# Kernel tuning notes

Hardware: AMD Instinct MI355X
Metric: run time of the kernel (lower is better)

Reference implementation:

```python
import jax, jax.numpy as jnp
import numpy as np

HEAD_SIZE = 64
NUM_HEADS = 16
D_MODEL = HEAD_SIZE * NUM_HEADS
BATCH = 2
SEQ = 2048


def setup_inputs() -> dict:
    key = jax.random.key(0)
    ks = jax.random.split(key, 9)
    s = 1.0 / np.sqrt(D_MODEL)
    inp = {
        "hidden_states": jax.random.normal(ks[0], (BATCH, SEQ, D_MODEL), jnp.float32),
        "Wq": jax.random.uniform(ks[1], (D_MODEL, D_MODEL), jnp.float32, -s, s),
        "bq": jax.random.uniform(ks[2], (D_MODEL,), jnp.float32, -s, s),
        "Wk": jax.random.uniform(ks[3], (D_MODEL, D_MODEL), jnp.float32, -s, s),
        "bk": jax.random.uniform(ks[4], (D_MODEL,), jnp.float32, -s, s),
        "Wv": jax.random.uniform(ks[5], (D_MODEL, D_MODEL), jnp.float32, -s, s),
        "bv": jax.random.uniform(ks[6], (D_MODEL,), jnp.float32, -s, s),
        "Wo": jax.random.uniform(ks[7], (D_MODEL, D_MODEL), jnp.float32, -s, s),
        "bo": jax.random.uniform(ks[8], (D_MODEL,), jnp.float32, -s, s),
    }
    return inp


def _split_heads(x):
    # [B, S, H*D] -> [B, H, S, D]
    b, s, _ = x.shape
    return x.reshape(b, s, NUM_HEADS, HEAD_SIZE).transpose(0, 2, 1, 3)


def reference(hidden_states, Wq, bq, Wk, bk, Wv, bv, Wo, bo):
    q = _split_heads(hidden_states @ Wq + bq)  # [B,H,S,D]
    k = _split_heads(hidden_states @ Wk + bk)
    v = _split_heads(hidden_states @ Wv + bv)
    scale = 1.0 / jnp.sqrt(jnp.asarray(HEAD_SIZE, hidden_states.dtype))
    scores = jnp.einsum("bhqd,bhkd->bhqk", q, k) * scale  # [B,H,S,S]
    weights = jax.nn.softmax(scores, axis=-1)
    attended = jnp.einsum("bhqk,bhkd->bhqd", weights, v)  # [B,H,S,D]
    merged = attended.transpose(0, 2, 1, 3).reshape(hidden_states.shape)  # [B,S,H*D]
    return merged @ Wo + bo
```

## Files before the change

kernel.cpp:

```cpp
#include <hip/hip_runtime.h>
#include <hip/hip_bf16.h>

#define D_MODEL 1024
#define HEADS 16
#define HSZ 64
#define BATCH 2
#define SEQ 2048
#define TOK (BATCH*SEQ)
#define NT (SEQ/64)

typedef __attribute__((ext_vector_type(8))) short bf16x8;
typedef __attribute__((ext_vector_type(4))) float f32x4;

#define QSCALE 0.1803368801111244f
#define THR_L2 11.541560327f

static __device__ __forceinline__ unsigned short f2bf(float f) {
  union { float f; unsigned u; } v; v.f = f;
  unsigned r = v.u + 0x7fffu + ((v.u >> 16) & 1u);
  return (unsigned short)(r >> 16);
}

static __device__ __forceinline__ float exp2_fast(float x) {
  float r;
  asm("v_exp_f32 %0, %1" : "=v"(r) : "v"(x));
  return r;
}

static __device__ __forceinline__ unsigned cvt_pk_bf16(float a, float b) {
  unsigned r;
  asm("v_cvt_pk_bf16_f32 %0, %1, %2" : "=v"(r) : "v"(a), "v"(b));
  return r;
}

static __device__ __forceinline__ int swz128(int row, int g) {
  return ((row << 7) + (g << 4)) ^ ((row & 7) << 4);
}

static __device__ __forceinline__ int xs4(int lr) {
  return ((lr & 7) << 1) | (lr >> 3);
}

static __device__ __forceinline__ void load_lds16(const void* g, void* l) {
  __builtin_amdgcn_global_load_lds(
      (const __attribute__((address_space(1))) unsigned*)g,
      (__attribute__((address_space(3))) unsigned*)l, 16, 0, 0);
}


__global__ void cvt_bf16_kernel(const float* __restrict__ src,
                                unsigned short* __restrict__ dst, int n) {
  int i = (blockIdx.x * blockDim.x + threadIdx.x) * 8;
  if (i >= n) return;
  float4 v0 = *reinterpret_cast<const float4*>(src + i);
  float4 v1 = *reinterpret_cast<const float4*>(src + i + 4);
  ushort4 o0, o1;
  o0.x = f2bf(v0.x); o0.y = f2bf(v0.y); o0.z = f2bf(v0.z); o0.w = f2bf(v0.w);
  o1.x = f2bf(v1.x); o1.y = f2bf(v1.y); o1.z = f2bf(v1.z); o1.w = f2bf(v1.w);
  *reinterpret_cast<ushort4*>(dst + i) = o0;
  *reinterpret_cast<ushort4*>(dst + i + 4) = o1;
}

__global__ void transpose_cvt_kernel(const float* __restrict__ Wq, const float* __restrict__ Wk,
                                     const float* __restrict__ Wv, const float* __restrict__ Wo,
                                     unsigned short* __restrict__ Wqkvt,
                                     unsigned short* __restrict__ Wot) {
  __shared__ float tile[32][33];
  int m = blockIdx.z;
  const float* src = (m == 0) ? Wq : (m == 1) ? Wk : (m == 2) ? Wv : Wo;
  unsigned short* dst = (m < 3) ? (Wqkvt + (size_t)m * D_MODEL * D_MODEL) : Wot;
  int i0 = blockIdx.y * 32, o0 = blockIdx.x * 32;
  int tx = threadIdx.x, ty = threadIdx.y;
  for (int k = 0; k < 32; k += 8)
    tile[ty + k][tx] = src[(size_t)(i0 + ty + k) * D_MODEL + o0 + tx];
  __syncthreads();
  for (int k = 0; k < 32; k += 8)
    dst[(size_t)(o0 + ty + k) * D_MODEL + i0 + tx] = f2bf(tile[tx][ty + k]);
}


template<int EPI>
__global__ __launch_bounds__(256) void gemm128_kernel(
    const unsigned short* __restrict__ A, const unsigned short* __restrict__ Bt,
    int K, int N,
    const float* __restrict__ b0, const float* __restrict__ b1, const float* __restrict__ b2,
    unsigned short* __restrict__ Qb, unsigned short* __restrict__ Kb,
    unsigned short* __restrict__ Vtb, float* __restrict__ Cout)
{
  __shared__ char As[128 * 64];
  __shared__ char Bs[128 * 64];
  int gx = gridDim.x;
  int orig = blockIdx.y * gx + blockIdx.x;
  int chunk = (gx * gridDim.y) >> 3;
  int sw = (orig & 7) * chunk + (orig >> 3);
  int m0 = (sw / gx) * 128, n0 = (sw % gx) * 128;
  int tid = threadIdx.x;
  int wv = tid >> 6, l = tid & 63;
  int wm = wv >> 1, wn = wv & 1;
  int lg = l >> 4, lr = l & 15;
  int srow = wv * 32 + (l >> 2);
  int scol = (l & 3) * 8;

  f32x4 acc[4][4];
#pragma unroll
  for (int i = 0; i < 4; i++)
#pragma unroll
    for (int j = 0; j < 4; j++) acc[i][j] = (f32x4){0.f, 0.f, 0.f, 0.f};

  for (int k0 = 0; k0 < K; k0 += 32) {
    __syncthreads();
    const unsigned short* ga = A  + (size_t)(m0 + srow) * K + k0 + scol;
    const unsigned short* gb = Bt + (size_t)(n0 + srow) * K + k0 + scol;
    load_lds16(ga,                       As + wv * 2048);
    load_lds16(ga + (size_t)16 * K,      As + wv * 2048 + 1024);
    load_lds16(gb,                       Bs + wv * 2048);
    load_lds16(gb + (size_t)16 * K,      Bs + wv * 2048 + 1024);
    __syncthreads();

    bf16x8 af[4], bfv[4];
#pragma unroll
    for (int mi = 0; mi < 4; mi++)
      af[mi] = *reinterpret_cast<const bf16x8*>(As + (wm * 64 + mi * 16 + lr) * 64 + lg * 16);
#pragma unroll
    for (int ni = 0; ni < 4; ni++)
      bfv[ni] = *reinterpret_cast<const bf16x8*>(Bs + (wn * 64 + ni * 16 + lr) * 64 + lg * 16);
#pragma unroll
    for (int mi = 0; mi < 4; mi++)
#pragma unroll
      for (int ni = 0; ni < 4; ni++)
        acc[mi][ni] = __builtin_amdgcn_mfma_f32_16x16x32_bf16(af[mi], bfv[ni], acc[mi][ni], 0, 0, 0);
  }

#pragma unroll
  for (int mi = 0; mi < 4; mi++) {
    int gr0 = m0 + wm * 64 + mi * 16 + lg * 4;
#pragma unroll
    for (int ni = 0; ni < 4; ni++) {
      int gc = n0 + wn * 64 + ni * 16 + lr;
      if (EPI == 0) {
        int mat = gc >> 10, o = gc & 1023;
        int hh = o >> 6, d = o & 63;
        const float* bias = (mat == 0) ? b0 : (mat == 1) ? b1 : b2;
        float bv = bias[o];
#pragma unroll
        for (int r = 0; r < 4; r++) {
          int t = gr0 + r;
          int b = t >> 11, s = t & 2047;
          float v = acc[mi][ni][r] + bv;
          if (mat == 0) v *= QSCALE;
          unsigned short u = f2bf(v);
          size_t head = (size_t)(b * HEADS + hh);
          if (mat == 0)
            Qb[(head * SEQ + s) * HSZ + d] = u;
          else if (mat == 1)
            Kb[((head * SEQ + s) * HSZ + d) ^ ((s & 7) << 3)] = u;
          else
            Vtb[(((head * HSZ + d) * SEQ + s)) ^ ((d & 7) << 3)] = u;
        }
      } else {
        float bv = b0[gc];
#pragma unroll
        for (int r = 0; r < 4; r++) {
          int t = gr0 + r;
          Cout[(size_t)t * N + gc] = acc[mi][ni][r] + bv;
        }
      }
    }
  }
}


#define KOFF(c) ((c) * 8192)
#define VOFF(c) (16384 + (c) * 8192)
#define POFF(w) (32768 + (w) * 2048)

__global__ __launch_bounds__(512, 4) void attn_kernel(
    const unsigned short* __restrict__ Qb, const unsigned short* __restrict__ Kb,
    const unsigned short* __restrict__ Vtb, unsigned short* __restrict__ Mg)
{
  __shared__ char lds[49152];

  int orig = blockIdx.y * 16 + blockIdx.x;
  int swzb = (orig & 7) * 64 + (orig >> 3);
  int bh = swzb >> 4;
  int q0 = (swzb & 15) * 128;
  int b = bh >> 4, h = bh & 15;
  int tid = threadIdx.x, w = tid >> 6, l = tid & 63;
  int lg = l >> 4, lr = l & 15;
  const unsigned short* Qh = Qb + (size_t)bh * SEQ * HSZ;
  const char* Kg = (const char*)(Kb + (size_t)bh * SEQ * HSZ) + (size_t)tid * 16;
  const char* Vg = (const char*)(Vtb + (size_t)bh * HSZ * SEQ)
                   + (size_t)(tid >> 3) * (SEQ * 2) + (tid & 7) * 16;

  int dsb[2] = { swz128(lr, lg), swz128(lr, lg + 4) };
  int pwa[4], paa[4];
#pragma unroll
  for (int ni = 0; ni < 4; ni++)
    pwa[ni] = POFF(w) + (lr << 7) + ((((ni << 2) + lg) ^ xs4(lr)) << 3);
#pragma unroll
  for (int k2 = 0; k2 < 2; k2++)
#pragma unroll
    for (int hh = 0; hh < 2; hh++)
      paa[k2 * 2 + hh] = POFF(w) + (lr << 7) + (((k2 * 8 + lg * 2 + hh) ^ xs4(lr)) << 3);

  bf16x8 qf2[2];
#pragma unroll
  for (int k2 = 0; k2 < 2; k2++)
    qf2[k2] = *reinterpret_cast<const bf16x8*>(
        Qh + (size_t)(q0 + w * 16 + lr) * HSZ + k2 * 32 + lg * 8);

  f32x4 of[4];
  f32x4 lones = (f32x4){0.f, 0.f, 0.f, 0.f};
#pragma unroll
  for (int ni = 0; ni < 4; ni++) of[ni] = (f32x4){0.f, 0.f, 0.f, 0.f};
  float m_r = -1e30f;

  bf16x8 vone;
#pragma unroll
  for (int j = 0; j < 8; j++) vone[j] = (short)0x3F80;

  auto stage = [&](int t, int nb) {
    if (t < NT) {
      load_lds16(Kg + (size_t)t * 8192, lds + KOFF(nb) + w * 1024);
      load_lds16(Vg + (size_t)t * 128,  lds + VOFF(nb) + w * 1024);
    }
  };

  auto body = [&](int t, int cur) {
    stage(t + 1, cur ^ 1);

    f32x4 sf[4];
#pragma unroll
    for (int ni = 0; ni < 4; ni++) {
      sf[ni] = (f32x4){0.f, 0.f, 0.f, 0.f};
#pragma unroll
      for (int k2 = 0; k2 < 2; k2++) {
        bf16x8 kf = *reinterpret_cast<const bf16x8*>(lds + dsb[k2] + KOFF(cur) + ni * 2048);
        sf[ni] = __builtin_amdgcn_mfma_f32_16x16x32_bf16(kf, qf2[k2], sf[ni], 0, 0, 0);
      }
    }

    float lm = fmaxf(fmaxf(fmaxf(sf[0][0], sf[0][1]), fmaxf(sf[0][2], sf[0][3])),
                     fmaxf(fmaxf(sf[1][0], sf[1][1]), fmaxf(sf[1][2], sf[1][3])));
    lm = fmaxf(lm,
         fmaxf(fmaxf(fmaxf(sf[2][0], sf[2][1]), fmaxf(sf[2][2], sf[2][3])),
               fmaxf(fmaxf(sf[3][0], sf[3][1]), fmaxf(sf[3][2], sf[3][3]))));

    if (__any(lm > m_r + THR_L2)) {
      float vm = fmaxf(lm, __shfl_xor(lm, 16));
      vm = fmaxf(vm, __shfl_xor(vm, 32));
      float mn = fmaxf(m_r, vm);
      float al = exp2_fast(m_r - mn);
      m_r = mn;
#pragma unroll
      for (int r = 0; r < 4; r++) {
        float a = __shfl(al, lg * 4 + r, 16);
        lones[r] *= a;
#pragma unroll
        for (int ni = 0; ni < 4; ni++) of[ni][r] *= a;
      }
    }

#pragma unroll
    for (int ni = 0; ni < 4; ni++) {
      uint2 pw;
      pw.x = cvt_pk_bf16(exp2_fast(sf[ni][0] - m_r), exp2_fast(sf[ni][1] - m_r));
      pw.y = cvt_pk_bf16(exp2_fast(sf[ni][2] - m_r), exp2_fast(sf[ni][3] - m_r));
      *reinterpret_cast<uint2*>(lds + pwa[ni]) = pw;
    }

    bf16x8 pa[2];
#pragma unroll
    for (int k2 = 0; k2 < 2; k2++) {
      uint2 lo = *reinterpret_cast<const uint2*>(lds + paa[k2 * 2]);
      uint2 hi = *reinterpret_cast<const uint2*>(lds + paa[k2 * 2 + 1]);
      int4 tt = {(int)lo.x, (int)lo.y, (int)hi.x, (int)hi.y};
      pa[k2] = *reinterpret_cast<bf16x8*>(&tt);
    }

    __builtin_amdgcn_s_setprio(1);
#pragma unroll
    for (int k2 = 0; k2 < 2; k2++)
      lones = __builtin_amdgcn_mfma_f32_16x16x32_bf16(pa[k2], vone, lones, 0, 0, 0);
#pragma unroll
    for (int ni = 0; ni < 4; ni++)
#pragma unroll
      for (int k2 = 0; k2 < 2; k2++) {
        bf16x8 vf = *reinterpret_cast<const bf16x8*>(lds + dsb[k2] + VOFF(cur) + ni * 2048);
        of[ni] = __builtin_amdgcn_mfma_f32_16x16x32_bf16(pa[k2], vf, of[ni], 0, 0, 0);
      }
    __builtin_amdgcn_s_setprio(0);

    __syncthreads();
  };

  stage(0, 0);
  __syncthreads();
  for (int kt = 0; kt < NT; kt += 2) {
    body(kt, 0);
    body(kt + 1, 1);
  }

#pragma unroll
  for (int r = 0; r < 4; r++) {
    float inv = 1.0f / lones[r];
    int q = q0 + w * 16 + lg * 4 + r;
#pragma unroll
    for (int ni = 0; ni < 4; ni++) {
      int dm = h * 64 + ni * 16 + lr;
      Mg[(size_t)(b * SEQ + q) * D_MODEL + dm] = f2bf(of[ni][r] * inv);
    }
  }
}


extern "C" void kernel_launch(void* const* d_in, const int* in_sizes, int n_in,
                              void* d_out, int out_size, void* d_ws, size_t ws_size,
                              hipStream_t stream) {
  const float* X  = (const float*)d_in[0];
  const float* Wq = (const float*)d_in[1];
  const float* bq = (const float*)d_in[2];
  const float* Wk = (const float*)d_in[3];
  const float* bk = (const float*)d_in[4];
  const float* Wv = (const float*)d_in[5];
  const float* bv = (const float*)d_in[6];
  const float* Wo = (const float*)d_in[7];
  const float* bo = (const float*)d_in[8];
  float* out = (float*)d_out;

  char* ws = (char*)d_ws;
  unsigned short* Xbf   = (unsigned short*)(ws);
  unsigned short* Wqkvt = (unsigned short*)(ws + ((size_t)8  << 20));
  unsigned short* Wot   = (unsigned short*)(ws + ((size_t)14 << 20));
  unsigned short* Qb    = (unsigned short*)(ws + ((size_t)16 << 20));
  unsigned short* Kb    = (unsigned short*)(ws + ((size_t)24 << 20));
  unsigned short* Vtb   = (unsigned short*)(ws + ((size_t)32 << 20));
  unsigned short* Mg = Xbf;

  cvt_bf16_kernel<<<(TOK * D_MODEL / 8 + 255) / 256, 256, 0, stream>>>(X, Xbf, TOK * D_MODEL);
  transpose_cvt_kernel<<<dim3(32, 32, 4), dim3(32, 8), 0, stream>>>(Wq, Wk, Wv, Wo, Wqkvt, Wot);
  gemm128_kernel<0><<<dim3(24, 32), 256, 0, stream>>>(Xbf, Wqkvt, 1024, 3072,
                                                      bq, bk, bv, Qb, Kb, Vtb, nullptr);
  attn_kernel<<<dim3(16, 32), 512, 0, stream>>>(Qb, Kb, Vtb, Mg);
  gemm128_kernel<1><<<dim3(8, 32), 256, 0, stream>>>(Mg, Wot, 1024, 1024,
                                                     bo, nullptr, nullptr,
                                                     nullptr, nullptr, nullptr, out);
}
```

Before: 203.7 us.

## Specialize QKV and projection GEMMs with K=64 XOR-swizzled tiles and staged V transpose

Splits the templated GEMM into a QKV kernel and an output-projection kernel. Both now load K-depth 64 per iteration into XOR-swizzled LDS to cut bank conflicts and halve barrier count. The QKV kernel stages the V tile through LDS so V^T is written with 16-byte coalesced stores instead of scattered 2-byte ones. The projection kernel uses 128x64 tiles for more blocks. This trades extra LDS and added complexity for better memory efficiency in both GEMMs.

```diff
diff --git a/kernel.cpp b/kernel.cpp
--- a/kernel.cpp
+++ b/kernel.cpp
@@ -79,16 +79,15 @@
 }
 
 
-template<int EPI>
-__global__ __launch_bounds__(256) void gemm128_kernel(
+__global__ __launch_bounds__(256, 3) void gemm_qkv_kernel(
     const unsigned short* __restrict__ A, const unsigned short* __restrict__ Bt,
-    int K, int N,
     const float* __restrict__ b0, const float* __restrict__ b1, const float* __restrict__ b2,
     unsigned short* __restrict__ Qb, unsigned short* __restrict__ Kb,
-    unsigned short* __restrict__ Vtb, float* __restrict__ Cout)
+    unsigned short* __restrict__ Vtb)
 {
-  __shared__ char As[128 * 64];
-  __shared__ char Bs[128 * 64];
+  __shared__ char As[16384];
+  __shared__ char Bs[16384];
+  const int K = D_MODEL;
   int gx = gridDim.x;
   int orig = blockIdx.y * gx + blockIdx.x;
   int chunk = (gx * gridDim.y) >> 3;
@@ -98,8 +97,16 @@
   int wv = tid >> 6, l = tid & 63;
   int wm = wv >> 1, wn = wv & 1;
   int lg = l >> 4, lr = l & 15;
-  int srow = wv * 32 + (l >> 2);
-  int scol = (l & 3) * 8;
+
+  int sr = wv * 32 + (l >> 3);
+  int csw = ((l & 7) ^ (l >> 3)) << 3;
+  const unsigned short* gaA = A  + (size_t)(m0 + sr) * K + csw;
+  const unsigned short* gaB = Bt + (size_t)(n0 + sr) * K + csw;
+
+  int gk0 = ((lg       ^ (lr & 7)) << 4);
+  int gk1 = (((4 + lg) ^ (lr & 7)) << 4);
+  int arow = (wm * 64 + lr) * 128;
+  int brow = (wn * 64 + lr) * 128;
 
   f32x4 acc[4][4];
 #pragma unroll
@@ -107,41 +114,45 @@
 #pragma unroll
     for (int j = 0; j < 4; j++) acc[i][j] = (f32x4){0.f, 0.f, 0.f, 0.f};
 
-  for (int k0 = 0; k0 < K; k0 += 32) {
-    __syncthreads();
-    const unsigned short* ga = A  + (size_t)(m0 + srow) * K + k0 + scol;
-    const unsigned short* gb = Bt + (size_t)(n0 + srow) * K + k0 + scol;
-    load_lds16(ga,                       As + wv * 2048);
-    load_lds16(ga + (size_t)16 * K,      As + wv * 2048 + 1024);
-    load_lds16(gb,                       Bs + wv * 2048);
-    load_lds16(gb + (size_t)16 * K,      Bs + wv * 2048 + 1024);
-    __syncthreads();
-
-    bf16x8 af[4], bfv[4];
+  for (int k0 = 0; k0 < K; k0 += 64) {
+    __syncthreads();
+#pragma unroll
+    for (int i = 0; i < 4; i++) {
+      load_lds16(gaA + k0 + i * 8 * K, As + wv * 4096 + i * 1024);
+      load_lds16(gaB + k0 + i * 8 * K, Bs + wv * 4096 + i * 1024);
+    }
+    __syncthreads();
+
+    bf16x8 af0[4], af1[4], bf0[4], bf1[4];
+#pragma unroll
+    for (int mi = 0; mi < 4; mi++) {
+      af0[mi] = *reinterpret_cast<const bf16x8*>(As + arow + mi * 2048 + gk0);
+      af1[mi] = *reinterpret_cast<const bf16x8*>(As + arow + mi * 2048 + gk1);
+    }
+#pragma unroll
+    for (int ni = 0; ni < 4; ni++) {
+      bf0[ni] = *reinterpret_cast<const bf16x8*>(Bs + brow + ni * 2048 + gk0);
+      bf1[ni] = *reinterpret_cast<const bf16x8*>(Bs + brow + ni * 2048 + gk1);
+    }
 #pragma unroll
     for (int mi = 0; mi < 4; mi++)
-      af[mi] = *reinterpret_cast<const bf16x8*>(As + (wm * 64 + mi * 16 + lr) * 64 + lg * 16);
-#pragma unroll
-    for (int ni = 0; ni < 4; ni++)
-      bfv[ni] = *reinterpret_cast<const bf16x8*>(Bs + (wn * 64 + ni * 16 + lr) * 64 + lg * 16);
-#pragma unroll
-    for (int mi = 0; mi < 4; mi++)
-#pragma unroll
-      for (int ni = 0; ni < 4; ni++)
-        acc[mi][ni] = __builtin_amdgcn_mfma_f32_16x16x32_bf16(af[mi], bfv[ni], acc[mi][ni], 0, 0, 0);
-  }
-
-#pragma unroll
-  for (int mi = 0; mi < 4; mi++) {
-    int gr0 = m0 + wm * 64 + mi * 16 + lg * 4;
-#pragma unroll
-    for (int ni = 0; ni < 4; ni++) {
-      int gc = n0 + wn * 64 + ni * 16 + lr;
-      if (EPI == 0) {
+#pragma unroll
+      for (int ni = 0; ni < 4; ni++) {
+        acc[mi][ni] = __builtin_amdgcn_mfma_f32_16x16x32_bf16(af0[mi], bf0[ni], acc[mi][ni], 0, 0, 0);
+        acc[mi][ni] = __builtin_amdgcn_mfma_f32_16x16x32_bf16(af1[mi], bf1[ni], acc[mi][ni], 0, 0, 0);
+      }
+  }
+
+  if (n0 < 2048) {
+#pragma unroll
+    for (int mi = 0; mi < 4; mi++) {
+      int gr0 = m0 + wm * 64 + mi * 16 + lg * 4;
+#pragma unroll
+      for (int ni = 0; ni < 4; ni++) {
+        int gc = n0 + wn * 64 + ni * 16 + lr;
         int mat = gc >> 10, o = gc & 1023;
         int hh = o >> 6, d = o & 63;
-        const float* bias = (mat == 0) ? b0 : (mat == 1) ? b1 : b2;
-        float bv = bias[o];
+        float bv = (mat == 0) ? b0[o] : b1[o];
 #pragma unroll
         for (int r = 0; r < 4; r++) {
           int t = gr0 + r;
@@ -152,19 +163,140 @@
           size_t head = (size_t)(b * HEADS + hh);
           if (mat == 0)
             Qb[(head * SEQ + s) * HSZ + d] = u;
-          else if (mat == 1)
+          else
             Kb[((head * SEQ + s) * HSZ + d) ^ ((s & 7) << 3)] = u;
-          else
-            Vtb[(((head * HSZ + d) * SEQ + s)) ^ ((d & 7) << 3)] = u;
         }
-      } else {
-        float bv = b0[gc];
-#pragma unroll
-        for (int r = 0; r < 4; r++) {
-          int t = gr0 + r;
-          Cout[(size_t)t * N + gc] = acc[mi][ni][r] + bv;
+      }
+    }
+  } else {
+    int bglob = m0 >> 11;
+    int hh0 = (n0 - 2048) >> 6;
+    float bvv[4];
+#pragma unroll
+    for (int ni = 0; ni < 4; ni++) bvv[ni] = b2[(n0 - 2048) + wn * 64 + ni * 16 + lr];
+
+    __syncthreads();
+    {
+      char* dstbuf = (wm == 0) ? As : Bs;
+#pragma unroll
+      for (int mi = 0; mi < 4; mi++) {
+        int lrow = mi * 16 + lg * 4;
+#pragma unroll
+        for (int ni = 0; ni < 4; ni++) {
+          int cc = wn * 64 + ni * 16 + lr;
+          uint2 pw;
+          pw.x = cvt_pk_bf16(acc[mi][ni][0] + bvv[ni], acc[mi][ni][1] + bvv[ni]);
+          pw.y = cvt_pk_bf16(acc[mi][ni][2] + bvv[ni], acc[mi][ni][3] + bvv[ni]);
+          int ba = (cc * 128 + lrow * 2) ^ ((cc & 7) << 3);
+          *reinterpret_cast<uint2*>(dstbuf + ba) = pw;
         }
       }
+    }
+    __syncthreads();
+    int ck = tid & 7;
+#pragma unroll
+    for (int pass = 0; pass < 4; ++pass) {
+      int cc = (tid >> 3) + pass * 32;
+      int x = cc & 7;
+      int d = cc & 63, hh = hh0 + (cc >> 6);
+      size_t rowbase = (((size_t)(bglob * HEADS + hh)) * HSZ + d) * SEQ;
+      int slo = ((ck * 2)     ^ x) << 3;
+      int shi = ((ck * 2 + 1) ^ x) << 3;
+      {
+        uint2 lo = *reinterpret_cast<const uint2*>(As + (cc << 7) + slo);
+        uint2 hi = *reinterpret_cast<const uint2*>(As + (cc << 7) + shi);
+        int s = (m0 & 2047) + ck * 8;
+        size_t idx = (rowbase + s) ^ ((d & 7) << 3);
+        uint4 val = {lo.x, lo.y, hi.x, hi.y};
+        *reinterpret_cast<uint4*>(Vtb + idx) = val;
+      }
+      {
+        uint2 lo = *reinterpret_cast<const uint2*>(Bs + (cc << 7) + slo);
+        uint2 hi = *reinterpret_cast<const uint2*>(Bs + (cc << 7) + shi);
+        int s = (m0 & 2047) + 64 + ck * 8;
+        size_t idx = (rowbase + s) ^ ((d & 7) << 3);
+        uint4 val = {lo.x, lo.y, hi.x, hi.y};
+        *reinterpret_cast<uint4*>(Vtb + idx) = val;
+      }
+    }
+  }
+}
+
+
+__global__ __launch_bounds__(256, 2) void gemm_proj_kernel(
+    const unsigned short* __restrict__ A, const unsigned short* __restrict__ Bt,
+    const float* __restrict__ bias, float* __restrict__ Cout)
+{
+  __shared__ char As[16384];
+  __shared__ char Bs[8192];
+  const int K = D_MODEL;
+  int gx = gridDim.x;
+  int orig = blockIdx.y * gx + blockIdx.x;
+  int chunk = (gx * gridDim.y) >> 3;
+  int sw = (orig & 7) * chunk + (orig >> 3);
+  int m0 = (sw / gx) * 128, n0 = (sw % gx) * 64;
+  int tid = threadIdx.x;
+  int wv = tid >> 6, l = tid & 63;
+  int wm = wv >> 1, wn = wv & 1;
+  int lg = l >> 4, lr = l & 15;
+
+  int srA = wv * 32 + (l >> 3);
+  int srB = wv * 16 + (l >> 3);
+  int csw = ((l & 7) ^ (l >> 3)) << 3;
+  const unsigned short* gaA = A  + (size_t)(m0 + srA) * K + csw;
+  const unsigned short* gaB = Bt + (size_t)(n0 + srB) * K + csw;
+
+  int gk0 = ((lg       ^ (lr & 7)) << 4);
+  int gk1 = (((4 + lg) ^ (lr & 7)) << 4);
+  int arow = (wm * 64 + lr) * 128;
+  int brow = (wn * 32 + lr) * 128;
+
+  f32x4 acc[4][2];
+#pragma unroll
+  for (int i = 0; i < 4; i++)
+#pragma unroll
+    for (int j = 0; j < 2; j++) acc[i][j] = (f32x4){0.f, 0.f, 0.f, 0.f};
+
+  for (int k0 = 0; k0 < K; k0 += 64) {
+    __syncthreads();
+#pragma unroll
+    for (int i = 0; i < 4; i++)
+      load_lds16(gaA + k0 + i * 8 * K, As + wv * 4096 + i * 1024);
+#pragma unroll
+    for (int i = 0; i < 2; i++)
+      load_lds16(gaB + k0 + i * 8 * K, Bs + wv * 2048 + i * 1024);
+    __syncthreads();
+
+    bf16x8 af0[4], af1[4], bf0[2], bf1[2];
+#pragma unroll
+    for (int mi = 0; mi < 4; mi++) {
+      af0[mi] = *reinterpret_cast<const bf16x8*>(As + arow + mi * 2048 + gk0);
+      af1[mi] = *reinterpret_cast<const bf16x8*>(As + arow + mi * 2048 + gk1);
+    }
+#pragma unroll
+    for (int ni = 0; ni < 2; ni++) {
+      bf0[ni] = *reinterpret_cast<const bf16x8*>(Bs + brow + ni * 2048 + gk0);
+      bf1[ni] = *reinterpret_cast<const bf16x8*>(Bs + brow + ni * 2048 + gk1);
+    }
+#pragma unroll
+    for (int mi = 0; mi < 4; mi++)
+#pragma unroll
+      for (int ni = 0; ni < 2; ni++) {
+        acc[mi][ni] = __builtin_amdgcn_mfma_f32_16x16x32_bf16(af0[mi], bf0[ni], acc[mi][ni], 0, 0, 0);
+        acc[mi][ni] = __builtin_amdgcn_mfma_f32_16x16x32_bf16(af1[mi], bf1[ni], acc[mi][ni], 0, 0, 0);
+      }
+  }
+
+#pragma unroll
+  for (int mi = 0; mi < 4; mi++) {
+    int gr0 = m0 + wm * 64 + mi * 16 + lg * 4;
+#pragma unroll
+    for (int ni = 0; ni < 2; ni++) {
+      int gc = n0 + wn * 32 + ni * 16 + lr;
+      float bv = bias[gc];
+#pragma unroll
+      for (int r = 0; r < 4; r++)
+        Cout[(size_t)(gr0 + r) * D_MODEL + gc] = acc[mi][ni][r] + bv;
     }
   }
 }
@@ -339,10 +471,7 @@
 
   cvt_bf16_kernel<<<(TOK * D_MODEL / 8 + 255) / 256, 256, 0, stream>>>(X, Xbf, TOK * D_MODEL);
   transpose_cvt_kernel<<<dim3(32, 32, 4), dim3(32, 8), 0, stream>>>(Wq, Wk, Wv, Wo, Wqkvt, Wot);
-  gemm128_kernel<0><<<dim3(24, 32), 256, 0, stream>>>(Xbf, Wqkvt, 1024, 3072,
-                                                      bq, bk, bv, Qb, Kb, Vtb, nullptr);
+  gemm_qkv_kernel<<<dim3(24, 32), 256, 0, stream>>>(Xbf, Wqkvt, bq, bk, bv, Qb, Kb, Vtb);
   attn_kernel<<<dim3(16, 32), 512, 0, stream>>>(Qb, Kb, Vtb, Mg);
-  gemm128_kernel<1><<<dim3(8, 32), 256, 0, stream>>>(Mg, Wot, 1024, 1024,
-                                                     bo, nullptr, nullptr,
-                                                     nullptr, nullptr, nullptr, out);
-}
+  gemm_proj_kernel<<<dim3(16, 32), 256, 0, stream>>>(Mg, Wot, bo, out);
+}
```

After: 183.1 us. -10.1%, faster.
